# Performance work log

Measured on AMD Instinct MI355X. Metric: run time of the kernel, lower is better.

The kernel has to match this reference:

```python
import jax, jax.numpy as jnp
import numpy as np

N = 20000      # nodes
DEG = 16       # neighbors per destination node
E = N * DEG    # edges
G = 16         # graphs in batch


def _glorot(k, shape):
    lim = float(np.sqrt(6.0 / (shape[0] + shape[1])))
    return jax.random.uniform(k, shape, jnp.float32, -lim, lim)


def setup_inputs() -> dict:
    key = jax.random.key(0)
    ks = jax.random.split(key, 16)
    pos = jax.random.normal(ks[0], (N, 3), jnp.float32)
    edge_src = jax.random.randint(ks[1], (E,), 0, N)               # random neighbors
    edge_dst = jnp.repeat(jnp.arange(N), DEG)                       # every node is a dst
    batch = (jnp.arange(N) * G) // N                                # 16 contiguous graphs
    inp = {
        "pos": pos, "edge_src": edge_src, "edge_dst": edge_dst, "batch": batch,
        # conv1: mlp Linear(3+3 -> 128), Linear(128 -> 128)
        "c1_W1": _glorot(ks[2], (6, 128)),   "c1_b1": jnp.zeros((128,), jnp.float32),
        "c1_W2": _glorot(ks[3], (128, 128)), "c1_b2": jnp.zeros((128,), jnp.float32),
        # conv2: mlp Linear(128+3 -> 256), Linear(256 -> 256)
        "c2_W1": _glorot(ks[4], (131, 256)), "c2_b1": jnp.zeros((256,), jnp.float32),
        "c2_W2": _glorot(ks[5], (256, 256)), "c2_b2": jnp.zeros((256,), jnp.float32),
        "fc1_W": _glorot(ks[6], (256, 256)), "fc1_b": jnp.zeros((256,), jnp.float32),
        "fc2_W": _glorot(ks[7], (256, 128)), "fc2_b": jnp.zeros((128,), jnp.float32),
        "lab_W": _glorot(ks[8], (128, 10)),  "lab_b": jnp.zeros((10,), jnp.float32),
        "box_W": _glorot(ks[9], (128, 6)),   "box_b": jnp.zeros((6,), jnp.float32),
    }
    return inp


def _pointnet_conv(x, pos, src, dst, W1, b1, W2, b2):
    # gather: x_j, pos_j - pos_i per edge
    rel = pos[src] - pos[dst]                          # [E, 3]
    msg = jnp.concatenate([x[src], rel], axis=-1)      # [E, Cin+3]
    h = jnp.maximum(msg @ W1 + b1, 0.0) @ W2 + b2      # [E, Cout]
    # scatter-max aggregation per destination node (all nodes covered)
    return jax.ops.segment_max(h, dst, num_segments=N)


def reference(pos, edge_src, edge_dst, batch,
              c1_W1, c1_b1, c1_W2, c1_b2,
              c2_W1, c2_b1, c2_W2, c2_b2,
              fc1_W, fc1_b, fc2_W, fc2_b,
              lab_W, lab_b, box_W, box_b):
    x = pos  # model uses data.pos as both x and pos
    x = _pointnet_conv(x, pos, edge_src, edge_dst, c1_W1, c1_b1, c1_W2, c1_b2)
    x = _pointnet_conv(x, pos, edge_src, edge_dst, c2_W1, c2_b1, c2_W2, c2_b2)
    x = jax.ops.segment_max(x, batch, num_segments=G)  # global_max_pool -> [G, 256]
    x = jnp.maximum(x @ fc1_W + fc1_b, 0.0)
    x = jnp.maximum(x @ fc2_W + fc2_b, 0.0)
    labels = x @ lab_W + lab_b                          # [G, 10]
    bbox = x @ box_W + box_b                            # [G, 6]
    return (labels, bbox)
```

## Files before the change

kernel.cpp:

```cpp
#include <hip/hip_runtime.h>

#define N_NODES 20000
#define DEG 16
#define GRAPHS 16
#define NPG 1250

typedef __bf16 bf16x8 __attribute__((ext_vector_type(8)));
typedef float f32x4 __attribute__((ext_vector_type(4)));
#define MFMA16(a, b, c) __builtin_amdgcn_mfma_f32_16x16x32_bf16(a, b, c, 0, 0, 0)

__device__ __forceinline__ void ldsbar() {
    __asm__ volatile("s_waitcnt lgkmcnt(0)\n\ts_barrier" ::: "memory");
}
__device__ __forceinline__ void async16(void* lds, const void* g) {
    __builtin_amdgcn_global_load_lds(
        (const __attribute__((address_space(1))) unsigned int*)(g),
        (__attribute__((address_space(3))) unsigned int*)(lds), 16, 0, 0);
}

#define OFF_X1    0
#define OFF_P1    2560000
#define OFF_P2    2564096
#define OFF_P3    2580480
#define OFF_P4    2621440
#define OFF_POOL_BYTES 5373952
#define OFF_MSGE  2695176
#define ZROW      320000

__global__ __launch_bounds__(256) void pack_weights(
    const float* __restrict__ c1W1, const float* __restrict__ c1W2,
    const float* __restrict__ c2W1, const float* __restrict__ c2W2,
    __bf16* __restrict__ p1, __bf16* __restrict__ p2,
    __bf16* __restrict__ p3, __bf16* __restrict__ p4,
    unsigned int* __restrict__ pooled, __bf16* __restrict__ msgE)
{
    int t = blockIdx.x * 256 + threadIdx.x;
    if (t < GRAPHS * 256) pooled[t] = 0u;
    if (t == 0) {
        bf16x8 z;
        #pragma unroll
        for (int j = 0; j < 8; j++) z[j] = (__bf16)0.f;
        *(bf16x8*)&msgE[(size_t)ZROW * 8] = z;
    }
    if (t >= 15872) return;
    const float* W; __bf16* out; int M, Kreal, KT, grp; bool c2w1 = false;
    if      (t <  512)  { W = c1W1; out = p1; M = 128; Kreal =   6; KT = 1; grp = t; }
    else if (t < 2560)  { W = c1W2; out = p2; M = 128; Kreal = 128; KT = 4; grp = t - 512; }
    else if (t < 7680)  { W = c2W1; out = p3; M = 256; Kreal = 131; KT = 5; grp = t - 2560; c2w1 = true; }
    else                { W = c2W2; out = p4; M = 256; Kreal = 256; KT = 8; grp = t - 7680; }
    int lane = grp & 63, rest = grp >> 6;
    int kt = rest % KT, mt = rest / KT;
    int m = mt * 16 + (lane & 15);
    int kbase = kt * 32 + ((lane >> 4) << 3);
    bf16x8 v;
    #pragma unroll
    for (int j = 0; j < 8; j++) {
        int ks = kbase + j;
        int wr;
        if (c2w1) wr = (ks < 128) ? ks : ((ks >= 131 && ks < 134) ? ks - 3 : -1);
        else      wr = (ks < Kreal) ? ks : -1;
        v[j] = (wr >= 0) ? (__bf16)W[wr * M + m] : (__bf16)0.f;
    }
    *(bf16x8*)&out[grp * 8] = v;
}

__global__ __launch_bounds__(256) void gatherE_kernel(
    const float* __restrict__ pos, const int* __restrict__ esrc,
    __bf16* __restrict__ msgE)
{
    int e = blockIdx.x * 256 + threadIdx.x;
    int d = e >> 4;
    int s = esrc[e];
    float sx = pos[3*s], sy = pos[3*s+1], sz = pos[3*s+2];
    float dx = pos[3*d], dy = pos[3*d+1], dz = pos[3*d+2];
    bf16x8 v;
    v[0] = (__bf16)sx; v[1] = (__bf16)sy; v[2] = (__bf16)sz;
    v[3] = (__bf16)(sx - dx); v[4] = (__bf16)(sy - dy); v[5] = (__bf16)(sz - dz);
    v[6] = (__bf16)0.f; v[7] = (__bf16)0.f;
    *(bf16x8*)&msgE[(size_t)e * 8] = v;
}

#define NB1T 4
#define NT1 10
__global__ __launch_bounds__(512, 4) void conv1_kernel(
    const __bf16* __restrict__ msgE,
    const __bf16* __restrict__ W1p, const float* __restrict__ b1,
    const __bf16* __restrict__ W2p, const float* __restrict__ b2,
    __bf16* __restrict__ x1)
{
    __shared__ __attribute__((aligned(16))) __bf16 msgF[3][NB1T * 64 * 8];
    __shared__ __attribute__((aligned(16))) __bf16 hidF[2][NB1T * 4 * 64 * 8];
    const int tid = threadIdx.x, lane = tid & 63, wave = tid >> 6;
    const int quad = lane >> 4, col = lane & 15;
    const int base = blockIdx.x * (NB1T * NT1);

    if (wave < 4) {
        bf16x8 A1[2];
        f32x4 bias1[2];
        #pragma unroll
        for (int i = 0; i < 2; i++) {
            int mtg = wave * 2 + i;
            A1[i] = *(const bf16x8*)&W1p[(mtg * 64 + lane) * 8];
            bias1[i] = *(const f32x4*)&b1[mtg * 16 + quad * 4];
        }
        auto stage = [&](int td, int buf) {
            int nl = wave;
            int row = (quad == 0) ? ((base + td * NB1T + nl) * 16 + col) : ZROW;
            async16(&msgF[buf][nl * 64 * 8], &msgE[(size_t)row * 8]);
        };
        stage(0, 0);
        stage(1, 1);
        for (int k = 0; k < NT1; k++) {
            int td = k + 2; if (td >= NT1) td -= NT1;
            stage(td, (k + 2) % 3);
            __asm__ volatile("s_waitcnt vmcnt(2)" ::: "memory");
            const int bufi = k % 3, bufo = k & 1;
            #pragma unroll
            for (int nl = 0; nl < NB1T; nl++) {
                bf16x8 B = *(const bf16x8*)&msgF[bufi][(nl * 64 + lane) * 8];
                #pragma unroll
                for (int i = 0; i < 2; i++) {
                    int mtg = wave * 2 + i;
                    f32x4 acc = bias1[i];
                    acc = MFMA16(A1[i], B, acc);
                    union { __bf16 h[4]; uint2 u; } pk;
                    #pragma unroll
                    for (int r = 0; r < 4; r++) pk.h[r] = (__bf16)fmaxf(acc[r], 0.f);
                    int kt2 = mtg >> 1;
                    int lane2 = ((mtg * 2 + (quad >> 1)) & 3) * 16 + col;
                    int j0 = (quad & 1) * 4;
                    *(uint2*)&hidF[bufo][((nl * 4 + kt2) * 64 + lane2) * 8 + j0] = pk.u;
                }
            }
            ldsbar();
        }
    } else {
        const int wv = wave - 4;
        bf16x8 B2w[2][4];
        float b2v[2];
        #pragma unroll
        for (int i = 0; i < 2; i++) {
            int mtg = wv * 2 + i;
            #pragma unroll
            for (int kt = 0; kt < 4; kt++)
                B2w[i][kt] = *(const bf16x8*)&W2p[((mtg * 4 + kt) * 64 + lane) * 8];
            b2v[i] = b2[mtg * 16 + col];
        }
        for (int k = 0; k < NT1; k++) {
            ldsbar();
            const int buf = k & 1;
            const int n0 = base + k * NB1T;
            #pragma unroll
            for (int nl = 0; nl < NB1T; nl++) {
                bf16x8 hA[4];
                #pragma unroll
                for (int kt = 0; kt < 4; kt++)
                    hA[kt] = *(const bf16x8*)&hidF[buf][((nl * 4 + kt) * 64 + lane) * 8];
                f32x4 acc[2];
                f32x4 z = {0.f, 0.f, 0.f, 0.f};
                acc[0] = z; acc[1] = z;
                #pragma unroll
                for (int kt = 0; kt < 4; kt++) {
                    #pragma unroll
                    for (int i = 0; i < 2; i++) acc[i] = MFMA16(hA[kt], B2w[i][kt], acc[i]);
                }
                #pragma unroll
                for (int i = 0; i < 2; i++) {
                    float m = fmaxf(fmaxf(acc[i][0], acc[i][1]), fmaxf(acc[i][2], acc[i][3]));
                    m = fmaxf(m, __shfl_xor(m, 16));
                    m = fmaxf(m, __shfl_xor(m, 32));
                    if (lane < 16)
                        x1[(size_t)(n0 + nl) * 128 + (wv * 2 + i) * 16 + lane] =
                            (__bf16)(m + b2v[i]);
                }
            }
        }
    }
}

#define NB2 2
#define NT2 20
__global__ __launch_bounds__(512) __attribute__((amdgpu_waves_per_eu(2, 2)))
void conv2_kernel(
    const int* __restrict__ esrc,
    const __bf16* __restrict__ x1, const __bf16* __restrict__ msgE,
    const __bf16* __restrict__ W1p, const float* __restrict__ b1,
    const __bf16* __restrict__ W2p, const float* __restrict__ b2,
    unsigned int* __restrict__ pooled)
{
    __shared__ __attribute__((aligned(16))) __bf16 msgF[3][NB2 * 5 * 64 * 8];
    __shared__ __attribute__((aligned(16))) __bf16 hidF[2][NB2 * 8 * 64 * 8];
    __shared__ int sSrc[NB2 * NT2 * 16];
    const int tid = threadIdx.x, lane = tid & 63, wave = tid >> 6;
    const int quad = lane >> 4, col = lane & 15;
    const int base = blockIdx.x * (NB2 * NT2);

    for (int u = tid; u < NB2 * NT2 * 16; u += 512) sSrc[u] = esrc[base * 16 + u];
    __syncthreads();

    if (wave < 4) {
        bf16x8 A1[4][5];
        f32x4 bias1[4];
        #pragma unroll
        for (int i = 0; i < 4; i++) {
            int tg = wave * 4 + i;
            #pragma unroll
            for (int kt = 0; kt < 5; kt++)
                A1[i][kt] = *(const bf16x8*)&W1p[((tg * 5 + kt) * 64 + lane) * 8];
            bias1[i] = *(const f32x4*)&b1[tg * 16 + quad * 4];
        }

        auto stage = [&](int td, int buf) {
            #pragma unroll
            for (int s = 0; s < 3; s++) {
                int g = wave + 4 * s;
                if (g < 10) {
                    int nl = g / 5, kt = g % 5;
                    __bf16* ldst = &msgF[buf][g * 64 * 8];
                    const __bf16* gsrc;
                    if (kt < 4) {
                        int src = sSrc[(td * NB2 + nl) * 16 + col];
                        gsrc = &x1[(size_t)src * 128 + kt * 32 + quad * 8];
                    } else {
                        int row = (quad == 0) ? ((base + td * NB2 + nl) * 16 + col) : ZROW;
                        gsrc = &msgE[(size_t)row * 8];
                    }
                    async16(ldst, gsrc);
                }
            }
        };

        stage(0, 0);
        stage(1, 1);

        for (int k = 0; k < NT2; k++) {
            int td = k + 2;
            if (td >= NT2) td -= NT2;
            stage(td, (k + 2) % 3);
            if (wave < 2) __asm__ volatile("s_waitcnt vmcnt(6)" ::: "memory");
            else          __asm__ volatile("s_waitcnt vmcnt(4)" ::: "memory");
            const int bufi = k % 3, bufo = k & 1;
            #pragma unroll
            for (int nl = 0; nl < NB2; nl++) {
                bf16x8 B[5];
                #pragma unroll
                for (int kt = 0; kt < 5; kt++)
                    B[kt] = *(const bf16x8*)&msgF[bufi][((nl * 5 + kt) * 64 + lane) * 8];
                #pragma unroll
                for (int i = 0; i < 4; i++) {
                    int mtg = wave * 4 + i;
                    f32x4 acc = bias1[i];
                    #pragma unroll
                    for (int kt = 0; kt < 5; kt++) acc = MFMA16(A1[i][kt], B[kt], acc);
                    union { __bf16 h[4]; uint2 u; } pk;
                    #pragma unroll
                    for (int r = 0; r < 4; r++) pk.h[r] = (__bf16)fmaxf(acc[r], 0.f);
                    int kt2 = mtg >> 1;
                    int lane2 = ((mtg * 2 + (quad >> 1)) & 3) * 16 + col;
                    int j0 = (quad & 1) * 4;
                    *(uint2*)&hidF[bufo][((nl * 8 + kt2) * 64 + lane2) * 8 + j0] = pk.u;
                }
            }
            ldsbar();
        }
    } else {
        const int wv = wave - 4;
        bf16x8 B2r[4][8];
        #pragma unroll
        for (int i = 0; i < 4; i++) {
            int tg = wv * 4 + i;
            #pragma unroll
            for (int kt = 0; kt < 8; kt++)
                B2r[i][kt] = *(const bf16x8*)&W2p[((tg * 8 + kt) * 64 + lane) * 8];
        }
        f32x4 runmax[4];
        #pragma unroll
        for (int i = 0; i < 4; i++)
            #pragma unroll
            for (int r = 0; r < 4; r++) runmax[i][r] = -3.4e38f;
        int gprev = base / NPG;

        auto flushfn = [&]() {
            #pragma unroll
            for (int i = 0; i < 4; i++) {
                float v = fmaxf(fmaxf(runmax[i][0], runmax[i][1]),
                                fmaxf(runmax[i][2], runmax[i][3]));
                v = fmaxf(v, __shfl_xor(v, 16));
                v = fmaxf(v, __shfl_xor(v, 32));
                if (lane < 16) {
                    int c = (wv * 4 + i) * 16 + lane;
                    float val = v + b2[c];
                    unsigned u = __float_as_uint(val);
                    u = (u & 0x80000000u) ? ~u : (u | 0x80000000u);
                    atomicMax(&pooled[gprev * 256 + c], u);
                }
                #pragma unroll
                for (int r = 0; r < 4; r++) runmax[i][r] = -3.4e38f;
            }
        };
        auto consume = [&](int tk) {
            int buf1 = tk & 1;
            int n0 = base + tk * NB2;
            #pragma unroll
            for (int nl = 0; nl < NB2; nl++) {
                int g = (n0 + nl) / NPG;
                if (g != gprev) { flushfn(); gprev = g; }
                bf16x8 hA[8];
                #pragma unroll
                for (int kt = 0; kt < 8; kt++)
                    hA[kt] = *(const bf16x8*)&hidF[buf1][((nl * 8 + kt) * 64 + lane) * 8];
                f32x4 acc[4];
                f32x4 z = {0.f, 0.f, 0.f, 0.f};
                #pragma unroll
                for (int i = 0; i < 4; i++) acc[i] = z;
                #pragma unroll
                for (int kt = 0; kt < 8; kt++) {
                    #pragma unroll
                    for (int i = 0; i < 4; i++) acc[i] = MFMA16(hA[kt], B2r[i][kt], acc[i]);
                }
                #pragma unroll
                for (int i = 0; i < 4; i++)
                    #pragma unroll
                    for (int r = 0; r < 4; r++)
                        runmax[i][r] = fmaxf(runmax[i][r], acc[i][r]);
            }
        };

        for (int k = 0; k < NT2; k++) {
            ldsbar();
            consume(k);
        }
        flushfn();
    }
}

__global__ __launch_bounds__(1024) void head_kernel(
    const unsigned int* __restrict__ pooled,
    const float* __restrict__ fc1_W, const float* __restrict__ fc1_b,
    const float* __restrict__ fc2_W, const float* __restrict__ fc2_b,
    const float* __restrict__ lab_W, const float* __restrict__ lab_b,
    const float* __restrict__ box_W, const float* __restrict__ box_b,
    float* __restrict__ out)
{
    __shared__ float p[256], h1s[256], h2s[128], red[1024];
    const int g = blockIdx.x, tid = threadIdx.x;
    if (tid < 256) {
        unsigned u = pooled[g * 256 + tid];
        u = (u & 0x80000000u) ? (u & 0x7fffffffu) : ~u;
        p[tid] = __uint_as_float(u);
    }
    __syncthreads();
    {
        int c = tid & 255, kq = tid >> 8;
        float a = 0.f;
        #pragma unroll 8
        for (int k0 = 0; k0 < 64; k0++) {
            int k = kq * 64 + k0;
            a += p[k] * fc1_W[k * 256 + c];
        }
        red[tid] = a;
    }
    __syncthreads();
    if (tid < 256)
        h1s[tid] = fmaxf(red[tid] + red[256 + tid] + red[512 + tid] + red[768 + tid]
                         + fc1_b[tid], 0.f);
    __syncthreads();
    if (tid < 512) {
        int c = tid & 127, kq = tid >> 7;
        float a = 0.f;
        #pragma unroll 8
        for (int k0 = 0; k0 < 64; k0++) {
            int k = kq * 64 + k0;
            a += h1s[k] * fc2_W[k * 128 + c];
        }
        red[tid] = a;
    }
    __syncthreads();
    if (tid < 128)
        h2s[tid] = fmaxf(red[tid] + red[128 + tid] + red[256 + tid] + red[384 + tid]
                         + fc2_b[tid], 0.f);
    __syncthreads();
    if (tid < 128) {
        int o = tid >> 3, kq = tid & 7;
        float a = 0.f;
        #pragma unroll
        for (int k0 = 0; k0 < 16; k0++) {
            int k = kq * 16 + k0;
            float w = (o < 10) ? lab_W[k * 10 + o] : box_W[k * 6 + (o - 10)];
            a += h2s[k] * w;
        }
        red[tid] = a;
    }
    __syncthreads();
    if (tid < 16) {
        float a = 0.f;
        #pragma unroll
        for (int q = 0; q < 8; q++) a += red[tid * 8 + q];
        if (tid < 10) out[g * 10 + tid] = a + lab_b[tid];
        else          out[160 + g * 6 + (tid - 10)] = a + box_b[tid - 10];
    }
}

extern "C" void kernel_launch(void* const* d_in, const int* in_sizes, int n_in,
                              void* d_out, int out_size, void* d_ws, size_t ws_size,
                              hipStream_t stream) {
    const float* pos   = (const float*)d_in[0];
    const int*   esrc  = (const int*)  d_in[1];
    const float* c1W1 = (const float*)d_in[4];
    const float* c1b1 = (const float*)d_in[5];
    const float* c1W2 = (const float*)d_in[6];
    const float* c1b2 = (const float*)d_in[7];
    const float* c2W1 = (const float*)d_in[8];
    const float* c2b1 = (const float*)d_in[9];
    const float* c2W2 = (const float*)d_in[10];
    const float* c2b2 = (const float*)d_in[11];
    const float* fc1W = (const float*)d_in[12];
    const float* fc1b = (const float*)d_in[13];
    const float* fc2W = (const float*)d_in[14];
    const float* fc2b = (const float*)d_in[15];
    const float* labW = (const float*)d_in[16];
    const float* labb = (const float*)d_in[17];
    const float* boxW = (const float*)d_in[18];
    const float* boxb = (const float*)d_in[19];

    __bf16* wsb = (__bf16*)d_ws;
    __bf16* x1   = wsb + OFF_X1;
    __bf16* p1   = wsb + OFF_P1;
    __bf16* p2   = wsb + OFF_P2;
    __bf16* p3   = wsb + OFF_P3;
    __bf16* p4   = wsb + OFF_P4;
    __bf16* msgE = wsb + OFF_MSGE;
    unsigned int* pooled = (unsigned int*)((char*)d_ws + OFF_POOL_BYTES);

    pack_weights<<<62, 256, 0, stream>>>(c1W1, c1W2, c2W1, c2W2, p1, p2, p3, p4, pooled, msgE);
    gatherE_kernel<<<1250, 256, 0, stream>>>(pos, esrc, msgE);
    conv1_kernel<<<N_NODES / (NB1T * NT1), 512, 0, stream>>>(msgE, p1, c1b1, p2, c1b2, x1);
    conv2_kernel<<<N_NODES / (NB2 * NT2), 512, 0, stream>>>(esrc, x1, msgE, p3, c2b1, p4, c2b2, pooled);
    head_kernel<<<GRAPHS, 1024, 0, stream>>>(pooled, fc1W, fc1b, fc2W, fc2b,
                                             labW, labb, boxW, boxb, (float*)d_out);
}
```

Baseline: 192.4 us.

## Fuse edge gather into weight packing; unify conv1 waves and enlarge conv2 tiles

Merges the edge-message gather kernel into the weight-packing kernel to remove one launch. Rewrites conv1 so all 8 waves run both MLP layers in sequence over a single hidden buffer, instead of splitting into producer and consumer waves, with 16 nodes per step and 5 steps. Conv2 now processes 4 nodes per tile instead of 2, which halves its grid and issues 5 async loads per wave per stage. The costs are more LDS and fewer blocks per CU for conv1, extra barriers, and less parallelism in conv2.

```diff
diff --git a/kernel.cpp b/kernel.cpp
--- a/kernel.cpp
+++ b/kernel.cpp
@@ -27,7 +27,8 @@
 #define OFF_MSGE  2695176
 #define ZROW      320000
 
-__global__ __launch_bounds__(256) void pack_weights(
+__global__ __launch_bounds__(256) void prep_kernel(
+    const float* __restrict__ pos, const int* __restrict__ esrc,
     const float* __restrict__ c1W1, const float* __restrict__ c1W2,
     const float* __restrict__ c2W1, const float* __restrict__ c2W2,
     __bf16* __restrict__ p1, __bf16* __restrict__ p2,
@@ -35,6 +36,17 @@
     unsigned int* __restrict__ pooled, __bf16* __restrict__ msgE)
 {
     int t = blockIdx.x * 256 + threadIdx.x;
+    {
+        int e = t, d = e >> 4;
+        int s = esrc[e];
+        float sx = pos[3*s], sy = pos[3*s+1], sz = pos[3*s+2];
+        float dx = pos[3*d], dy = pos[3*d+1], dz = pos[3*d+2];
+        bf16x8 v;
+        v[0] = (__bf16)sx; v[1] = (__bf16)sy; v[2] = (__bf16)sz;
+        v[3] = (__bf16)(sx - dx); v[4] = (__bf16)(sy - dy); v[5] = (__bf16)(sz - dz);
+        v[6] = (__bf16)0.f; v[7] = (__bf16)0.f;
+        *(bf16x8*)&msgE[(size_t)e * 8] = v;
+    }
     if (t < GRAPHS * 256) pooled[t] = 0u;
     if (t == 0) {
         bf16x8 z;
@@ -64,121 +76,79 @@
     *(bf16x8*)&out[grp * 8] = v;
 }
 
-__global__ __launch_bounds__(256) void gatherE_kernel(
-    const float* __restrict__ pos, const int* __restrict__ esrc,
-    __bf16* __restrict__ msgE)
-{
-    int e = blockIdx.x * 256 + threadIdx.x;
-    int d = e >> 4;
-    int s = esrc[e];
-    float sx = pos[3*s], sy = pos[3*s+1], sz = pos[3*s+2];
-    float dx = pos[3*d], dy = pos[3*d+1], dz = pos[3*d+2];
-    bf16x8 v;
-    v[0] = (__bf16)sx; v[1] = (__bf16)sy; v[2] = (__bf16)sz;
-    v[3] = (__bf16)(sx - dx); v[4] = (__bf16)(sy - dy); v[5] = (__bf16)(sz - dz);
-    v[6] = (__bf16)0.f; v[7] = (__bf16)0.f;
-    *(bf16x8*)&msgE[(size_t)e * 8] = v;
-}
-
-#define NB1T 4
-#define NT1 10
-__global__ __launch_bounds__(512, 4) void conv1_kernel(
+#define NB1T 16
+#define NT1 5
+__global__ __launch_bounds__(512, 2) void conv1_kernel(
     const __bf16* __restrict__ msgE,
     const __bf16* __restrict__ W1p, const float* __restrict__ b1,
     const __bf16* __restrict__ W2p, const float* __restrict__ b2,
     __bf16* __restrict__ x1)
 {
     __shared__ __attribute__((aligned(16))) __bf16 msgF[3][NB1T * 64 * 8];
-    __shared__ __attribute__((aligned(16))) __bf16 hidF[2][NB1T * 4 * 64 * 8];
+    __shared__ __attribute__((aligned(16))) __bf16 hidF[NB1T * 4 * 64 * 8];
     const int tid = threadIdx.x, lane = tid & 63, wave = tid >> 6;
     const int quad = lane >> 4, col = lane & 15;
     const int base = blockIdx.x * (NB1T * NT1);
 
-    if (wave < 4) {
-        bf16x8 A1[2];
-        f32x4 bias1[2];
-        #pragma unroll
-        for (int i = 0; i < 2; i++) {
-            int mtg = wave * 2 + i;
-            A1[i] = *(const bf16x8*)&W1p[(mtg * 64 + lane) * 8];
-            bias1[i] = *(const f32x4*)&b1[mtg * 16 + quad * 4];
-        }
-        auto stage = [&](int td, int buf) {
-            int nl = wave;
+    bf16x8 A1 = *(const bf16x8*)&W1p[(wave * 64 + lane) * 8];
+    f32x4 bias1 = *(const f32x4*)&b1[wave * 16 + quad * 4];
+    bf16x8 B2w[4];
+    #pragma unroll
+    for (int kt = 0; kt < 4; kt++)
+        B2w[kt] = *(const bf16x8*)&W2p[((wave * 4 + kt) * 64 + lane) * 8];
+    float b2v = b2[wave * 16 + col];
+
+    auto stage = [&](int td, int buf) {
+        #pragma unroll
+        for (int s = 0; s < 2; s++) {
+            int nl = wave * 2 + s;
             int row = (quad == 0) ? ((base + td * NB1T + nl) * 16 + col) : ZROW;
             async16(&msgF[buf][nl * 64 * 8], &msgE[(size_t)row * 8]);
-        };
-        stage(0, 0);
-        stage(1, 1);
-        for (int k = 0; k < NT1; k++) {
-            int td = k + 2; if (td >= NT1) td -= NT1;
-            stage(td, (k + 2) % 3);
-            __asm__ volatile("s_waitcnt vmcnt(2)" ::: "memory");
-            const int bufi = k % 3, bufo = k & 1;
-            #pragma unroll
-            for (int nl = 0; nl < NB1T; nl++) {
-                bf16x8 B = *(const bf16x8*)&msgF[bufi][(nl * 64 + lane) * 8];
-                #pragma unroll
-                for (int i = 0; i < 2; i++) {
-                    int mtg = wave * 2 + i;
-                    f32x4 acc = bias1[i];
-                    acc = MFMA16(A1[i], B, acc);
-                    union { __bf16 h[4]; uint2 u; } pk;
-                    #pragma unroll
-                    for (int r = 0; r < 4; r++) pk.h[r] = (__bf16)fmaxf(acc[r], 0.f);
-                    int kt2 = mtg >> 1;
-                    int lane2 = ((mtg * 2 + (quad >> 1)) & 3) * 16 + col;
-                    int j0 = (quad & 1) * 4;
-                    *(uint2*)&hidF[bufo][((nl * 4 + kt2) * 64 + lane2) * 8 + j0] = pk.u;
-                }
-            }
-            ldsbar();
-        }
-    } else {
-        const int wv = wave - 4;
-        bf16x8 B2w[2][4];
-        float b2v[2];
-        #pragma unroll
-        for (int i = 0; i < 2; i++) {
-            int mtg = wv * 2 + i;
+        }
+    };
+    stage(0, 0);
+    stage(1, 1);
+
+    for (int k = 0; k < NT1; k++) {
+        int td = k + 2; if (td >= NT1) td -= NT1;
+        stage(td, (k + 2) % 3);
+        __asm__ volatile("s_waitcnt vmcnt(4)" ::: "memory");
+        const int bufi = k % 3;
+        #pragma unroll
+        for (int nl = 0; nl < NB1T; nl++) {
+            bf16x8 B = *(const bf16x8*)&msgF[bufi][(nl * 64 + lane) * 8];
+            f32x4 acc = bias1;
+            acc = MFMA16(A1, B, acc);
+            union { __bf16 h[4]; uint2 u; } pk;
+            #pragma unroll
+            for (int r = 0; r < 4; r++) pk.h[r] = (__bf16)fmaxf(acc[r], 0.f);
+            int kt2 = wave >> 1;
+            int lane2 = ((wave * 2 + (quad >> 1)) & 3) * 16 + col;
+            int j0 = (quad & 1) * 4;
+            *(uint2*)&hidF[((nl * 4 + kt2) * 64 + lane2) * 8 + j0] = pk.u;
+        }
+        ldsbar();
+        const int n0 = base + k * NB1T;
+        #pragma unroll
+        for (int nl = 0; nl < NB1T; nl++) {
+            bf16x8 hA[4];
             #pragma unroll
             for (int kt = 0; kt < 4; kt++)
-                B2w[i][kt] = *(const bf16x8*)&W2p[((mtg * 4 + kt) * 64 + lane) * 8];
-            b2v[i] = b2[mtg * 16 + col];
-        }
-        for (int k = 0; k < NT1; k++) {
-            ldsbar();
-            const int buf = k & 1;
-            const int n0 = base + k * NB1T;
-            #pragma unroll
-            for (int nl = 0; nl < NB1T; nl++) {
-                bf16x8 hA[4];
-                #pragma unroll
-                for (int kt = 0; kt < 4; kt++)
-                    hA[kt] = *(const bf16x8*)&hidF[buf][((nl * 4 + kt) * 64 + lane) * 8];
-                f32x4 acc[2];
-                f32x4 z = {0.f, 0.f, 0.f, 0.f};
-                acc[0] = z; acc[1] = z;
-                #pragma unroll
-                for (int kt = 0; kt < 4; kt++) {
-                    #pragma unroll
-                    for (int i = 0; i < 2; i++) acc[i] = MFMA16(hA[kt], B2w[i][kt], acc[i]);
-                }
-                #pragma unroll
-                for (int i = 0; i < 2; i++) {
-                    float m = fmaxf(fmaxf(acc[i][0], acc[i][1]), fmaxf(acc[i][2], acc[i][3]));
-                    m = fmaxf(m, __shfl_xor(m, 16));
-                    m = fmaxf(m, __shfl_xor(m, 32));
-                    if (lane < 16)
-                        x1[(size_t)(n0 + nl) * 128 + (wv * 2 + i) * 16 + lane] =
-                            (__bf16)(m + b2v[i]);
-                }
-            }
-        }
-    }
-}
-
-#define NB2 2
+                hA[kt] = *(const bf16x8*)&hidF[((nl * 4 + kt) * 64 + lane) * 8];
+            f32x4 acc = {0.f, 0.f, 0.f, 0.f};
+            #pragma unroll
+            for (int kt = 0; kt < 4; kt++) acc = MFMA16(hA[kt], B2w[kt], acc);
+            float m = fmaxf(fmaxf(acc[0], acc[1]), fmaxf(acc[2], acc[3]));
+            m = fmaxf(m, __shfl_xor(m, 16));
+            m = fmaxf(m, __shfl_xor(m, 32));
+            if (lane < 16)
+                x1[(size_t)(n0 + nl) * 128 + wave * 16 + lane] = (__bf16)(m + b2v);
+        }
+        ldsbar();
+    }
+}
+
+#define NB2 4
 #define NT2 20
 __global__ __launch_bounds__(512) __attribute__((amdgpu_waves_per_eu(2, 2)))
 void conv2_kernel(
@@ -212,21 +182,19 @@
 
         auto stage = [&](int td, int buf) {
             #pragma unroll
-            for (int s = 0; s < 3; s++) {
+            for (int s = 0; s < 5; s++) {
                 int g = wave + 4 * s;
-                if (g < 10) {
-                    int nl = g / 5, kt = g % 5;
-                    __bf16* ldst = &msgF[buf][g * 64 * 8];
-                    const __bf16* gsrc;
-                    if (kt < 4) {
-                        int src = sSrc[(td * NB2 + nl) * 16 + col];
-                        gsrc = &x1[(size_t)src * 128 + kt * 32 + quad * 8];
-                    } else {
-                        int row = (quad == 0) ? ((base + td * NB2 + nl) * 16 + col) : ZROW;
-                        gsrc = &msgE[(size_t)row * 8];
-                    }
-                    async16(ldst, gsrc);
+                int nl = g / 5, kt = g % 5;
+                __bf16* ldst = &msgF[buf][g * 64 * 8];
+                const __bf16* gsrc;
+                if (kt < 4) {
+                    int src = sSrc[(td * NB2 + nl) * 16 + col];
+                    gsrc = &x1[(size_t)src * 128 + kt * 32 + quad * 8];
+                } else {
+                    int row = (quad == 0) ? ((base + td * NB2 + nl) * 16 + col) : ZROW;
+                    gsrc = &msgE[(size_t)row * 8];
                 }
+                async16(ldst, gsrc);
             }
         };
 
@@ -237,8 +205,7 @@
             int td = k + 2;
             if (td >= NT2) td -= NT2;
             stage(td, (k + 2) % 3);
-            if (wave < 2) __asm__ volatile("s_waitcnt vmcnt(6)" ::: "memory");
-            else          __asm__ volatile("s_waitcnt vmcnt(4)" ::: "memory");
+            __asm__ volatile("s_waitcnt vmcnt(10)" ::: "memory");
             const int bufi = k % 3, bufo = k & 1;
             #pragma unroll
             for (int nl = 0; nl < NB2; nl++) {
@@ -432,8 +399,8 @@
     __bf16* msgE = wsb + OFF_MSGE;
     unsigned int* pooled = (unsigned int*)((char*)d_ws + OFF_POOL_BYTES);
 
-    pack_weights<<<62, 256, 0, stream>>>(c1W1, c1W2, c2W1, c2W2, p1, p2, p3, p4, pooled, msgE);
-    gatherE_kernel<<<1250, 256, 0, stream>>>(pos, esrc, msgE);
+    prep_kernel<<<1250, 256, 0, stream>>>(pos, esrc, c1W1, c1W2, c2W1, c2W2,
+                                          p1, p2, p3, p4, pooled, msgE);
     conv1_kernel<<<N_NODES / (NB1T * NT1), 512, 0, stream>>>(msgE, p1, c1b1, p2, c1b2, x1);
     conv2_kernel<<<N_NODES / (NB2 * NT2), 512, 0, stream>>>(esrc, x1, msgE, p3, c2b1, p4, c2b2, pooled);
     head_kernel<<<GRAPHS, 1024, 0, stream>>>(pooled, fc1W, fc1b, fc2W, fc2b,
```

Measured after the change: 182.9 us. 4.9% less time.
